# Kernel optimization log

Measured on AMD Instinct MI355X. Metric: run time of the kernel, lower is better.

Reference implementation:

```python
import jax, jax.numpy as jnp
import numpy as np

N, E, D = 50000, 800000, 128
EPS = 1e-5  # PyG BatchNorm default eps


def setup_inputs() -> dict:
    key = jax.random.key(0)
    ks = jax.random.split(key, 12)
    s = 1.0 / np.sqrt(D)
    x = jax.random.normal(ks[0], (N, D), jnp.float32)
    edge_index = jax.random.randint(ks[1], (2, E), 0, N, dtype=jnp.int32)
    Wp = jax.random.normal(ks[2], (D, D), jnp.float32) * s
    bp = jax.random.normal(ks[3], (D,), jnp.float32) * 0.01
    # 4 SAGEConv layers, all 128->128, stacked: lin_l (neighbor, with bias) and lin_r (root)
    Wl = jax.random.normal(ks[4], (4, D, D), jnp.float32) * s
    bl = jax.random.normal(ks[5], (4, D), jnp.float32) * 0.01
    Wr = jax.random.normal(ks[6], (4, D, D), jnp.float32) * s
    # BatchNorm params/buffers (eval mode: running stats)
    bn_gamma = 1.0 + 0.1 * jax.random.normal(ks[7], (4, D), jnp.float32)
    bn_beta = 0.1 * jax.random.normal(ks[8], (4, D), jnp.float32)
    bn_mean = 0.1 * jax.random.normal(ks[9], (4, D), jnp.float32)
    bn_var = jax.random.uniform(ks[10], (4, D), jnp.float32, 0.5, 1.5)
    return {"x": x, "edge_index": edge_index, "Wp": Wp, "bp": bp, "Wl": Wl,
            "bl": bl, "Wr": Wr, "bn_gamma": bn_gamma, "bn_beta": bn_beta,
            "bn_mean": bn_mean, "bn_var": bn_var}


def _sage_conv(x, src, dst, inv_deg, Wl, bl, Wr):
    # mean-aggregate neighbor features: gather x[src], scatter-sum to dst, divide by degree
    agg = jax.ops.segment_sum(x[src], dst, num_segments=N) * inv_deg  # [N, D]
    # PyG SAGEConv: lin_l(aggr) + lin_r(x_root)
    return agg @ Wl + bl + x @ Wr


def _bn(h, gamma, beta, mean, var):
    return (h - mean) * (gamma * jax.lax.rsqrt(var + EPS)) + beta


def reference(x, edge_index, Wp, bp, Wl, bl, Wr, bn_gamma, bn_beta, bn_mean, bn_var):
    src, dst = edge_index[0], edge_index[1]
    deg = jax.ops.segment_sum(jnp.ones((E,), x.dtype), dst, num_segments=N)
    inv_deg = (1.0 / jnp.maximum(deg, 1.0))[:, None]  # [N, 1]
    x = jax.nn.relu(x @ Wp + bp)
    # eval mode: dropout is identity, BN uses running stats
    for i in range(3):
        h = _sage_conv(x, src, dst, inv_deg, Wl[i], bl[i], Wr[i])
        h = jax.nn.relu(_bn(h, bn_gamma[i], bn_beta[i], bn_mean[i], bn_var[i]))
        x = x + h
    x = _sage_conv(x, src, dst, inv_deg, Wl[3], bl[3], Wr[3])
    return jax.nn.relu(_bn(x, bn_gamma[3], bn_beta[3], bn_mean[3], bn_var[3]))
```

## Files before the change

### kernel.cpp

```cpp
#include <hip/hip_runtime.h>

#define DIM 128
#define BN_EPS 1e-5f
#define BCAP 8192
#define EPB 4096
#define EPT 16

typedef __bf16 bf16x8 __attribute__((ext_vector_type(8)));
typedef float f32x4 __attribute__((ext_vector_type(4)));
typedef float f32x2 __attribute__((ext_vector_type(2)));

__device__ __forceinline__ float bf_e0(unsigned int u) {
    return __builtin_bit_cast(float, u << 16);
}
__device__ __forceinline__ float bf_e1(unsigned int u) {
    return __builtin_bit_cast(float, u & 0xffff0000u);
}
__device__ __forceinline__ unsigned short f2b(float f) {
    __bf16 b = (__bf16)f;
    return __builtin_bit_cast(unsigned short, b);
}
__device__ __forceinline__ unsigned int pack2(float lo, float hi) {
    return (unsigned int)f2b(lo) | ((unsigned int)f2b(hi) << 16);
}

#define GLOAD_LDS16(gsrc, ldst)                                               \
    __builtin_amdgcn_global_load_lds(                                         \
        (const __attribute__((address_space(1))) void*)(gsrc),                \
        (__attribute__((address_space(3))) void*)(ldst), 16, 0, 0)

__global__ __launch_bounds__(256) void k_bin(const int* __restrict__ src,
                                             const int* __restrict__ dst,
                                             int* __restrict__ cursor,
                                             unsigned int* __restrict__ binned,
                                             const float* __restrict__ Wp,
                                             const float* __restrict__ Wl,
                                             const float* __restrict__ Wr,
                                             unsigned short* __restrict__ WTf,
                                             int E, int NB) {
    __shared__ int hist[256];
    __shared__ int base[256];
    __shared__ int c2[256];
    const int tid = threadIdx.x;
    const int e0 = blockIdx.x * EPB;

    unsigned int u[EPT];
    int b[EPT];
    hist[tid] = 0;
    c2[tid] = 0;
    __syncthreads();
#pragma unroll
    for (int i = 0; i < EPT; ++i) {
        int e = e0 + i * 256 + tid;
        if (e < E) {
            int d = dst[e];
            b[i] = d >> 8;
            u[i] = ((unsigned int)(d & 255) << 17) | (unsigned int)src[e];
            atomicAdd(&hist[b[i]], 1);
        } else {
            b[i] = -1;
        }
    }
    __syncthreads();
    if (tid < NB && hist[tid] > 0) base[tid] = atomicAdd(&cursor[tid], hist[tid]);
    __syncthreads();
#pragma unroll
    for (int i = 0; i < EPT; ++i) {
        if (b[i] < 0) continue;
        int p = base[b[i]] + atomicAdd(&c2[b[i]], 1);
        if (p < BCAP) binned[(size_t)b[i] * BCAP + p] = u[i];
    }

    int gid = blockIdx.x * 256 + tid;
    if (gid < 9 * 2048) {
        int m = gid >> 11;
        int r = gid & 2047;
        int lane = r & 63;
        int k = (r >> 6) & 3;
        int ct = r >> 8;
        int feat = ct * 16 + (lane & 15);
        int kb = k * 32 + (lane >> 4) * 8;
        const float* W = (m == 0) ? Wp : (m < 5) ? (Wl + (size_t)(m - 1) * DIM * DIM)
                                                 : (Wr + (size_t)(m - 5) * DIM * DIM);
        unsigned short o[8];
#pragma unroll
        for (int e = 0; e < 8; ++e) o[e] = f2b(W[(size_t)(kb + e) * DIM + feat]);
        *(uint4*)(WTf + (size_t)gid * 8) = *(const uint4*)o;
    }
}

__global__ __launch_bounds__(256) void k_csr(const int* __restrict__ cursor,
                                             const unsigned int* __restrict__ binned,
                                             int* __restrict__ rowptr,
                                             float* __restrict__ inv_deg,
                                             int* __restrict__ col, int N, int NB) {
    __shared__ unsigned int stage[BCAP];
    __shared__ int deg[256];
    __shared__ int start[256];
    __shared__ int sh[256];
    const int b = blockIdx.x;
    const int t = threadIdx.x;
    const int node0 = b << 8;

    int v = (t < NB) ? min(cursor[t], BCAP) : 0;
    sh[t] = v;
    deg[t] = 0;
    __syncthreads();
    for (int off = 1; off < 256; off <<= 1) {
        int a = (t >= off) ? sh[t - off] : 0;
        __syncthreads();
        sh[t] += a;
        __syncthreads();
    }
    const int gbase = sh[b] - min(cursor[b], BCAP);
    const int cnt = min(cursor[b], BCAP);
    if (b == 0 && t == 255) rowptr[N] = sh[255];

    for (int e = t; e < cnt; e += 256) {
        unsigned int u = binned[(size_t)b * BCAP + e];
        stage[e] = u;
        atomicAdd(&deg[u >> 17], 1);
    }
    __syncthreads();
    int d = deg[t];
    start[t] = d;
    __syncthreads();
    for (int off = 1; off < 256; off <<= 1) {
        int a = (t >= off) ? start[t - off] : 0;
        __syncthreads();
        start[t] += a;
        __syncthreads();
    }
    int excl = start[t] - d;
    int node = node0 + t;
    if (node < N) {
        rowptr[node] = gbase + excl;
        inv_deg[node] = 1.0f / (float)(d > 1 ? d : 1);
    }
    __syncthreads();
    deg[t] = excl;
    __syncthreads();
    for (int e = t; e < cnt; e += 256) {
        unsigned int u = stage[e];
        int dl = u >> 17;
        int p = atomicAdd(&deg[dl], 1);
        col[gbase + p] = (int)(u & 0x1ffffu);
    }
}

__global__ void k_agg(const uint2* __restrict__ x8_2, const int* __restrict__ rowptr,
                      const int* __restrict__ col, const float* __restrict__ inv_deg,
                      uint4* __restrict__ aggb4, int n) {
    int node = (blockIdx.x * blockDim.x + threadIdx.x) >> 6;
    int lane = threadIdx.x & 63;
    if (node >= n) return;
    const int e4 = lane >> 4, c16 = lane & 15;
    const int lo = rowptr[node], hi = rowptr[node + 1];

    float a0 = 0.f, a1 = 0.f, a2 = 0.f, a3 = 0.f,
          a4 = 0.f, a5 = 0.f, a6 = 0.f, a7 = 0.f;

    int i0 = lo + e4;
    int s0 = (i0      < hi) ? col[i0]      : -1;
    int s1 = (i0 + 4  < hi) ? col[i0 + 4]  : -1;
    int s2 = (i0 + 8  < hi) ? col[i0 + 8]  : -1;
    int s3 = (i0 + 12 < hi) ? col[i0 + 12] : -1;

    for (int j = lo; j < hi; j += 16) {
        uint2 v0 = x8_2[(size_t)(s0 > 0 ? s0 : 0) * 16 + c16];
        uint2 v1 = x8_2[(size_t)(s1 > 0 ? s1 : 0) * 16 + c16];
        uint2 v2 = x8_2[(size_t)(s2 > 0 ? s2 : 0) * 16 + c16];
        uint2 v3 = x8_2[(size_t)(s3 > 0 ? s3 : 0) * 16 + c16];
        float m0 = s0 >= 0 ? 1.f : 0.f;
        float m1 = s1 >= 0 ? 1.f : 0.f;
        float m2 = s2 >= 0 ? 1.f : 0.f;
        float m3 = s3 >= 0 ? 1.f : 0.f;
        int nj = j + 16 + e4;
        s0 = (nj      < hi) ? col[nj]      : -1;
        s1 = (nj + 4  < hi) ? col[nj + 4]  : -1;
        s2 = (nj + 8  < hi) ? col[nj + 8]  : -1;
        s3 = (nj + 12 < hi) ? col[nj + 12] : -1;
#define ACC_(v, m)                                                            \
        {                                                                     \
            f32x2 f01 = __builtin_amdgcn_cvt_pk_f32_fp8(v.x, false);          \
            f32x2 f23 = __builtin_amdgcn_cvt_pk_f32_fp8(v.x, true);           \
            f32x2 f45 = __builtin_amdgcn_cvt_pk_f32_fp8(v.y, false);          \
            f32x2 f67 = __builtin_amdgcn_cvt_pk_f32_fp8(v.y, true);           \
            a0 = fmaf(f01.x, m, a0); a1 = fmaf(f01.y, m, a1);                 \
            a2 = fmaf(f23.x, m, a2); a3 = fmaf(f23.y, m, a3);                 \
            a4 = fmaf(f45.x, m, a4); a5 = fmaf(f45.y, m, a5);                 \
            a6 = fmaf(f67.x, m, a6); a7 = fmaf(f67.y, m, a7);                 \
        }
        ACC_(v0, m0) ACC_(v1, m1) ACC_(v2, m2) ACC_(v3, m3)
#undef ACC_
    }
#define RED_(a) a += __shfl_xor(a, 16); a += __shfl_xor(a, 32);
    RED_(a0) RED_(a1) RED_(a2) RED_(a3) RED_(a4) RED_(a5) RED_(a6) RED_(a7)
#undef RED_
    float sc = inv_deg[node];
    uint4 o;
    o.x = pack2(a0 * sc, a1 * sc);
    o.y = pack2(a2 * sc, a3 * sc);
    o.z = pack2(a4 * sc, a5 * sc);
    o.w = pack2(a6 * sc, a7 * sc);
    if (lane < 16) aggb4[(size_t)node * 16 + c16] = o;
}

template <int NSEG, bool A0F32>
__global__ __launch_bounds__(256) void k_gemm(
    const void* __restrict__ A0v, const unsigned short* __restrict__ A1,
    const unsigned short* __restrict__ Wf0, const unsigned short* __restrict__ Wf1,
    const float* __restrict__ bias,
    const float* __restrict__ gamma, const float* __restrict__ beta,
    const float* __restrict__ mean, const float* __restrict__ var,
    const unsigned short* __restrict__ residb,
    float* __restrict__ out32, unsigned short* __restrict__ outb,
    unsigned char* __restrict__ out8, int nrows) {
    __shared__ unsigned short wlds[16384];
    __shared__ float colp[2 * DIM];

    const int tid = threadIdx.x;
    const int lane = tid & 63;
    const int l15 = lane & 15;
    const int lhi = lane >> 4;
    const int wave = tid >> 6;
    const int node = blockIdx.x * 64 + wave * 16 + l15;
    const int arow = node < nrows ? node : nrows - 1;

    bf16x8 af0[4];
    if (A0F32) {
        const float* a0 = (const float*)A0v + (size_t)arow * DIM + lhi * 8;
#pragma unroll
        for (int k = 0; k < 4; ++k) {
            float4 v0 = *(const float4*)(a0 + k * 32);
            float4 v1 = *(const float4*)(a0 + k * 32 + 4);
            bf16x8 f;
            f[0] = (__bf16)v0.x; f[1] = (__bf16)v0.y;
            f[2] = (__bf16)v0.z; f[3] = (__bf16)v0.w;
            f[4] = (__bf16)v1.x; f[5] = (__bf16)v1.y;
            f[6] = (__bf16)v1.z; f[7] = (__bf16)v1.w;
            af0[k] = f;
        }
    } else {
        const unsigned short* a0 = (const unsigned short*)A0v + (size_t)arow * DIM + lhi * 8;
#pragma unroll
        for (int k = 0; k < 4; ++k) af0[k] = *(const bf16x8*)(a0 + k * 32);
    }

    {
        const unsigned short* g = Wf0 + (size_t)wave * 4096 + lane * 8;
#pragma unroll
        for (int i = 0; i < 8; ++i)
            GLOAD_LDS16(g + i * 512, &wlds[wave * 4096 + i * 512]);
    }

    if (tid < DIM) {
        float sc, sh;
        if (gamma) {
            float s = gamma[tid] * rsqrtf(var[tid] + BN_EPS);
            sc = s;
            sh = (bias[tid] - mean[tid]) * s + beta[tid];
        } else {
            sc = 1.f;
            sh = bias[tid];
        }
        colp[tid * 2] = sc;
        colp[tid * 2 + 1] = sh;
    }

    f32x4 acc[8];
#pragma unroll
    for (int ct = 0; ct < 8; ++ct) acc[ct] = (f32x4){0.f, 0.f, 0.f, 0.f};

    __syncthreads();

    bf16x8 af1[4];
    if (NSEG == 2) {
        const unsigned short* a1 = A1 + (size_t)arow * DIM + lhi * 8;
#pragma unroll
        for (int k = 0; k < 4; ++k) af1[k] = *(const bf16x8*)(a1 + k * 32);
    }

#pragma unroll
    for (int k = 0; k < 4; ++k) {
        bf16x8 bw[8];
#pragma unroll
        for (int ct = 0; ct < 8; ++ct)
            bw[ct] = *(const bf16x8*)&wlds[((ct * 4 + k) * 64 + lane) * 8];
#pragma unroll
        for (int ct = 0; ct < 8; ++ct)
            acc[ct] = __builtin_amdgcn_mfma_f32_16x16x32_bf16(bw[ct], af0[k],
                                                              acc[ct], 0, 0, 0);
    }

    if (NSEG == 2) {
        __syncthreads();
        {
            const unsigned short* g = Wf1 + (size_t)wave * 4096 + lane * 8;
#pragma unroll
            for (int i = 0; i < 8; ++i)
                GLOAD_LDS16(g + i * 512, &wlds[wave * 4096 + i * 512]);
        }
        __syncthreads();
#pragma unroll
        for (int k = 0; k < 4; ++k) {
            bf16x8 bw[8];
#pragma unroll
            for (int ct = 0; ct < 8; ++ct)
                bw[ct] = *(const bf16x8*)&wlds[((ct * 4 + k) * 64 + lane) * 8];
#pragma unroll
            for (int ct = 0; ct < 8; ++ct)
                acc[ct] = __builtin_amdgcn_mfma_f32_16x16x32_bf16(bw[ct], af1[k],
                                                                  acc[ct], 0, 0, 0);
        }
    }

    if (node < nrows) {
#pragma unroll
        for (int ct = 0; ct < 8; ++ct) {
            int c0 = ct * 16 + lhi * 4;
            float h[4];
#pragma unroll
            for (int j = 0; j < 4; ++j) {
                float2 p = *(const float2*)&colp[(c0 + j) * 2];
                h[j] = fmaxf(acc[ct][j] * p.x + p.y, 0.f);
            }
            size_t base = (size_t)node * DIM + c0;
            if (residb) {
                uint2 rv = *(const uint2*)(residb + base);
                h[0] += bf_e0(rv.x); h[1] += bf_e1(rv.x);
                h[2] += bf_e0(rv.y); h[3] += bf_e1(rv.y);
            }
            if (outb) {
                uint2 o;
                o.x = pack2(h[0], h[1]);
                o.y = pack2(h[2], h[3]);
                *(uint2*)(outb + base) = o;
            }
            if (out8) {
                int w = __builtin_amdgcn_cvt_pk_fp8_f32(h[0], h[1], 0, false);
                w = __builtin_amdgcn_cvt_pk_fp8_f32(h[2], h[3], w, true);
                *(unsigned int*)(out8 + base) = (unsigned int)w;
            }
            if (out32)
                *(float4*)(out32 + base) = make_float4(h[0], h[1], h[2], h[3]);
        }
    }
}

extern "C" void kernel_launch(void* const* d_in, const int* in_sizes, int n_in,
                              void* d_out, int out_size, void* d_ws, size_t ws_size,
                              hipStream_t stream) {
    const float* x_in = (const float*)d_in[0];
    const int* ei     = (const int*)d_in[1];
    const float* Wp   = (const float*)d_in[2];
    const float* bp   = (const float*)d_in[3];
    const float* Wl   = (const float*)d_in[4];
    const float* bl   = (const float*)d_in[5];
    const float* Wr   = (const float*)d_in[6];
    const float* g    = (const float*)d_in[7];
    const float* be   = (const float*)d_in[8];
    const float* mu   = (const float*)d_in[9];
    const float* va   = (const float*)d_in[10];

    const int N = in_sizes[0] / DIM;
    const int E = in_sizes[1] / 2;
    const int* src = ei;
    const int* dst = ei + E;
    const int NB = (N + 255) >> 8;

    char* p = (char*)d_ws;
    auto alloc = [&](size_t bytes) {
        char* r = p;
        p += (bytes + 255) & ~(size_t)255;
        return r;
    };
    float* inv_deg = (float*)alloc((size_t)N * 4);
    int* rowptr    = (int*)alloc((size_t)(N + 1) * 4);
    int* cursor    = (int*)alloc((size_t)NB * 4);
    int* col       = (int*)alloc((size_t)E * 4);
    unsigned int* binned = (unsigned int*)alloc((size_t)NB * BCAP * 4);
    unsigned short* xb   = (unsigned short*)alloc((size_t)N * DIM * 2);
    unsigned char* x8    = (unsigned char*)alloc((size_t)N * DIM);
    unsigned short* aggb = (unsigned short*)alloc((size_t)N * DIM * 2);
    unsigned short* WTf  = (unsigned short*)alloc((size_t)9 * 16384 * 2);

    hipMemsetAsync(cursor, 0, (size_t)NB * 4, stream);
    k_bin<<<(E + EPB - 1) / EPB, 256, 0, stream>>>(src, dst, cursor, binned,
                                                   Wp, Wl, Wr, WTf, E, NB);
    k_csr<<<NB, 256, 0, stream>>>(cursor, binned, rowptr, inv_deg, col, N, NB);

    const int gblocks = (N + 63) / 64;

    k_gemm<1, true><<<gblocks, 256, 0, stream>>>(
        x_in, nullptr, WTf, nullptr, bp,
        nullptr, nullptr, nullptr, nullptr, nullptr,
        nullptr, xb, x8, N);

    float* out = (float*)d_out;
    for (int i = 0; i < 4; ++i) {
        k_agg<<<(N + 3) / 4, 256, 0, stream>>>((const uint2*)x8, rowptr, col,
                                               inv_deg, (uint4*)aggb, N);
        const unsigned short* WlF = WTf + (size_t)(1 + i) * 16384;
        const unsigned short* WrF = WTf + (size_t)(5 + i) * 16384;
        k_gemm<2, false><<<gblocks, 256, 0, stream>>>(
            aggb, xb, WlF, WrF, bl + i * DIM,
            g + i * DIM, be + i * DIM, mu + i * DIM, va + i * DIM,
            (i < 3) ? xb : nullptr,
            (i < 3) ? nullptr : out, (i < 3) ? xb : nullptr,
            (i < 3) ? x8 : nullptr, N);
    }
}
```

Measured before the change: 209.6 us.

## Fuse neighbor aggregation into per-layer SAGE GEMM kernel with ping-pong fp8 buffers

Replaces the separate aggregation kernel and two-segment GEMM with one per-layer kernel. Each wave first gathers and mean-aggregates 16 nodes, two at a time, into a swizzled LDS tile, then runs the Wl and Wr MFMAs. Weights are read straight from global memory instead of being staged in LDS. This removes the bf16 aggregate round-trip to memory and one launch per layer, and the fp8 feature buffer is now double-buffered to avoid a read-write race. The cost is far fewer waves for the latency-bound gather (16 nodes per wave instead of one), plus possible imbalance from pairing nodes of different degree.

Result: slower. 318.3 us (+51.8%).

```diff
diff --git a/kernel.cpp b/kernel.cpp
--- a/kernel.cpp
+++ b/kernel.cpp
@@ -148,76 +148,12 @@
     }
 }
 
-__global__ void k_agg(const uint2* __restrict__ x8_2, const int* __restrict__ rowptr,
-                      const int* __restrict__ col, const float* __restrict__ inv_deg,
-                      uint4* __restrict__ aggb4, int n) {
-    int node = (blockIdx.x * blockDim.x + threadIdx.x) >> 6;
-    int lane = threadIdx.x & 63;
-    if (node >= n) return;
-    const int e4 = lane >> 4, c16 = lane & 15;
-    const int lo = rowptr[node], hi = rowptr[node + 1];
-
-    float a0 = 0.f, a1 = 0.f, a2 = 0.f, a3 = 0.f,
-          a4 = 0.f, a5 = 0.f, a6 = 0.f, a7 = 0.f;
-
-    int i0 = lo + e4;
-    int s0 = (i0      < hi) ? col[i0]      : -1;
-    int s1 = (i0 + 4  < hi) ? col[i0 + 4]  : -1;
-    int s2 = (i0 + 8  < hi) ? col[i0 + 8]  : -1;
-    int s3 = (i0 + 12 < hi) ? col[i0 + 12] : -1;
-
-    for (int j = lo; j < hi; j += 16) {
-        uint2 v0 = x8_2[(size_t)(s0 > 0 ? s0 : 0) * 16 + c16];
-        uint2 v1 = x8_2[(size_t)(s1 > 0 ? s1 : 0) * 16 + c16];
-        uint2 v2 = x8_2[(size_t)(s2 > 0 ? s2 : 0) * 16 + c16];
-        uint2 v3 = x8_2[(size_t)(s3 > 0 ? s3 : 0) * 16 + c16];
-        float m0 = s0 >= 0 ? 1.f : 0.f;
-        float m1 = s1 >= 0 ? 1.f : 0.f;
-        float m2 = s2 >= 0 ? 1.f : 0.f;
-        float m3 = s3 >= 0 ? 1.f : 0.f;
-        int nj = j + 16 + e4;
-        s0 = (nj      < hi) ? col[nj]      : -1;
-        s1 = (nj + 4  < hi) ? col[nj + 4]  : -1;
-        s2 = (nj + 8  < hi) ? col[nj + 8]  : -1;
-        s3 = (nj + 12 < hi) ? col[nj + 12] : -1;
-#define ACC_(v, m)                                                            \
-        {                                                                     \
-            f32x2 f01 = __builtin_amdgcn_cvt_pk_f32_fp8(v.x, false);          \
-            f32x2 f23 = __builtin_amdgcn_cvt_pk_f32_fp8(v.x, true);           \
-            f32x2 f45 = __builtin_amdgcn_cvt_pk_f32_fp8(v.y, false);          \
-            f32x2 f67 = __builtin_amdgcn_cvt_pk_f32_fp8(v.y, true);           \
-            a0 = fmaf(f01.x, m, a0); a1 = fmaf(f01.y, m, a1);                 \
-            a2 = fmaf(f23.x, m, a2); a3 = fmaf(f23.y, m, a3);                 \
-            a4 = fmaf(f45.x, m, a4); a5 = fmaf(f45.y, m, a5);                 \
-            a6 = fmaf(f67.x, m, a6); a7 = fmaf(f67.y, m, a7);                 \
-        }
-        ACC_(v0, m0) ACC_(v1, m1) ACC_(v2, m2) ACC_(v3, m3)
-#undef ACC_
-    }
-#define RED_(a) a += __shfl_xor(a, 16); a += __shfl_xor(a, 32);
-    RED_(a0) RED_(a1) RED_(a2) RED_(a3) RED_(a4) RED_(a5) RED_(a6) RED_(a7)
-#undef RED_
-    float sc = inv_deg[node];
-    uint4 o;
-    o.x = pack2(a0 * sc, a1 * sc);
-    o.y = pack2(a2 * sc, a3 * sc);
-    o.z = pack2(a4 * sc, a5 * sc);
-    o.w = pack2(a6 * sc, a7 * sc);
-    if (lane < 16) aggb4[(size_t)node * 16 + c16] = o;
-}
-
-template <int NSEG, bool A0F32>
-__global__ __launch_bounds__(256) void k_gemm(
-    const void* __restrict__ A0v, const unsigned short* __restrict__ A1,
-    const unsigned short* __restrict__ Wf0, const unsigned short* __restrict__ Wf1,
+__global__ __launch_bounds__(256) void k_proj(
+    const float* __restrict__ Ain, const unsigned short* __restrict__ Wf,
     const float* __restrict__ bias,
-    const float* __restrict__ gamma, const float* __restrict__ beta,
-    const float* __restrict__ mean, const float* __restrict__ var,
-    const unsigned short* __restrict__ residb,
-    float* __restrict__ out32, unsigned short* __restrict__ outb,
-    unsigned char* __restrict__ out8, int nrows) {
+    unsigned short* __restrict__ outb, unsigned char* __restrict__ out8,
+    int nrows) {
     __shared__ unsigned short wlds[16384];
-    __shared__ float colp[2 * DIM];
 
     const int tid = threadIdx.x;
     const int lane = tid & 63;
@@ -227,9 +163,9 @@
     const int node = blockIdx.x * 64 + wave * 16 + l15;
     const int arow = node < nrows ? node : nrows - 1;
 
-    bf16x8 af0[4];
-    if (A0F32) {
-        const float* a0 = (const float*)A0v + (size_t)arow * DIM + lhi * 8;
+    bf16x8 af[4];
+    {
+        const float* a0 = Ain + (size_t)arow * DIM + lhi * 8;
 #pragma unroll
         for (int k = 0; k < 4; ++k) {
             float4 v0 = *(const float4*)(a0 + k * 32);
@@ -239,47 +175,21 @@
             f[2] = (__bf16)v0.z; f[3] = (__bf16)v0.w;
             f[4] = (__bf16)v1.x; f[5] = (__bf16)v1.y;
             f[6] = (__bf16)v1.z; f[7] = (__bf16)v1.w;
-            af0[k] = f;
-        }
-    } else {
-        const unsigned short* a0 = (const unsigned short*)A0v + (size_t)arow * DIM + lhi * 8;
-#pragma unroll
-        for (int k = 0; k < 4; ++k) af0[k] = *(const bf16x8*)(a0 + k * 32);
-    }
-
+            af[k] = f;
+        }
+    }
     {
-        const unsigned short* g = Wf0 + (size_t)wave * 4096 + lane * 8;
+        const unsigned short* g = Wf + (size_t)wave * 4096 + lane * 8;
 #pragma unroll
         for (int i = 0; i < 8; ++i)
             GLOAD_LDS16(g + i * 512, &wlds[wave * 4096 + i * 512]);
     }
 
-    if (tid < DIM) {
-        float sc, sh;
-        if (gamma) {
-            float s = gamma[tid] * rsqrtf(var[tid] + BN_EPS);
-            sc = s;
-            sh = (bias[tid] - mean[tid]) * s + beta[tid];
-        } else {
-            sc = 1.f;
-            sh = bias[tid];
-        }
-        colp[tid * 2] = sc;
-        colp[tid * 2 + 1] = sh;
-    }
-
     f32x4 acc[8];
 #pragma unroll
     for (int ct = 0; ct < 8; ++ct) acc[ct] = (f32x4){0.f, 0.f, 0.f, 0.f};
 
     __syncthreads();
-
-    bf16x8 af1[4];
-    if (NSEG == 2) {
-        const unsigned short* a1 = A1 + (size_t)arow * DIM + lhi * 8;
-#pragma unroll
-        for (int k = 0; k < 4; ++k) af1[k] = *(const bf16x8*)(a1 + k * 32);
-    }
 
 #pragma unroll
     for (int k = 0; k < 4; ++k) {
@@ -289,33 +199,179 @@
             bw[ct] = *(const bf16x8*)&wlds[((ct * 4 + k) * 64 + lane) * 8];
 #pragma unroll
         for (int ct = 0; ct < 8; ++ct)
+            acc[ct] = __builtin_amdgcn_mfma_f32_16x16x32_bf16(bw[ct], af[k],
+                                                              acc[ct], 0, 0, 0);
+    }
+
+    if (node < nrows) {
+#pragma unroll
+        for (int ct = 0; ct < 8; ++ct) {
+            int c0 = ct * 16 + lhi * 4;
+            float4 bb = *(const float4*)(bias + c0);
+            float h[4];
+            h[0] = fmaxf(acc[ct][0] + bb.x, 0.f);
+            h[1] = fmaxf(acc[ct][1] + bb.y, 0.f);
+            h[2] = fmaxf(acc[ct][2] + bb.z, 0.f);
+            h[3] = fmaxf(acc[ct][3] + bb.w, 0.f);
+            size_t base = (size_t)node * DIM + c0;
+            uint2 o;
+            o.x = pack2(h[0], h[1]);
+            o.y = pack2(h[2], h[3]);
+            *(uint2*)(outb + base) = o;
+            int w = __builtin_amdgcn_cvt_pk_fp8_f32(h[0], h[1], 0, false);
+            w = __builtin_amdgcn_cvt_pk_fp8_f32(h[2], h[3], w, true);
+            *(unsigned int*)(out8 + base) = (unsigned int)w;
+        }
+    }
+}
+
+__global__ __launch_bounds__(256) void k_layer(
+    const uint2* __restrict__ x8in, const unsigned short* __restrict__ xb,
+    const int* __restrict__ rowptr, const int* __restrict__ col,
+    const float* __restrict__ inv_deg,
+    const unsigned short* __restrict__ Wl, const unsigned short* __restrict__ Wr,
+    const float* __restrict__ bias, const float* __restrict__ gamma,
+    const float* __restrict__ beta, const float* __restrict__ mean,
+    const float* __restrict__ var,
+    unsigned short* __restrict__ outb, unsigned char* __restrict__ out8,
+    float* __restrict__ out32, int nrows) {
+    __shared__ uint4 atile[4][16][16];
+    __shared__ float colp[2 * DIM];
+
+    const int tid = threadIdx.x;
+    const int lane = tid & 63;
+    const int wave = tid >> 6;
+    const int l15 = lane & 15;
+    const int lhi = lane >> 4;
+    const int e4 = lhi, c16 = l15;
+    const int nbase = blockIdx.x * 64 + wave * 16;
+
+    if (tid < DIM) {
+        float s = gamma[tid] * rsqrtf(var[tid] + BN_EPS);
+        colp[tid * 2] = s;
+        colp[tid * 2 + 1] = (bias[tid] - mean[tid]) * s + beta[tid];
+    }
+
+#define PRIME4(S0, S1, S2, S3, base_, hi_)                                    \
+    S0 = ((base_) < (hi_)) ? col[(base_)] : -1;                               \
+    S1 = ((base_) + 4 < (hi_)) ? col[(base_) + 4] : -1;                       \
+    S2 = ((base_) + 8 < (hi_)) ? col[(base_) + 8] : -1;                       \
+    S3 = ((base_) + 12 < (hi_)) ? col[(base_) + 12] : -1;
+
+#define CVT8ACC(v, m, Q0, Q1, Q2, Q3, Q4, Q5, Q6, Q7)                         \
+    {                                                                         \
+        f32x2 f01 = __builtin_amdgcn_cvt_pk_f32_fp8((v).x, false);            \
+        f32x2 f23 = __builtin_amdgcn_cvt_pk_f32_fp8((v).x, true);             \
+        f32x2 f45 = __builtin_amdgcn_cvt_pk_f32_fp8((v).y, false);            \
+        f32x2 f67 = __builtin_amdgcn_cvt_pk_f32_fp8((v).y, true);             \
+        Q0 = fmaf(f01.x, m, Q0); Q1 = fmaf(f01.y, m, Q1);                     \
+        Q2 = fmaf(f23.x, m, Q2); Q3 = fmaf(f23.y, m, Q3);                     \
+        Q4 = fmaf(f45.x, m, Q4); Q5 = fmaf(f45.y, m, Q5);                     \
+        Q6 = fmaf(f67.x, m, Q6); Q7 = fmaf(f67.y, m, Q7);                     \
+    }
+
+#define RED2(q) q += __shfl_xor(q, 16); q += __shfl_xor(q, 32);
+
+    for (int i = 0; i < 16; i += 2) {
+        const int nA = nbase + i, nB = nbase + i + 1;
+        float A0 = 0.f, A1 = 0.f, A2 = 0.f, A3 = 0.f,
+              A4 = 0.f, A5 = 0.f, A6 = 0.f, A7 = 0.f;
+        float B0 = 0.f, B1 = 0.f, B2 = 0.f, B3 = 0.f,
+              B4 = 0.f, B5 = 0.f, B6 = 0.f, B7 = 0.f;
+        int loA = 0, hiA = 0, loB = 0, hiB = 0;
+        if (nA < nrows) { loA = rowptr[nA]; hiA = rowptr[nA + 1]; }
+        if (nB < nrows) { loB = rowptr[nB]; hiB = rowptr[nB + 1]; }
+        int sA0, sA1, sA2, sA3, sB0, sB1, sB2, sB3;
+        PRIME4(sA0, sA1, sA2, sA3, loA + e4, hiA)
+        PRIME4(sB0, sB1, sB2, sB3, loB + e4, hiB)
+        for (int jA = loA, jB = loB; jA < hiA || jB < hiB; jA += 16, jB += 16) {
+            uint2 vA0 = x8in[(size_t)(sA0 > 0 ? sA0 : 0) * 16 + c16];
+            uint2 vA1 = x8in[(size_t)(sA1 > 0 ? sA1 : 0) * 16 + c16];
+            uint2 vA2 = x8in[(size_t)(sA2 > 0 ? sA2 : 0) * 16 + c16];
+            uint2 vA3 = x8in[(size_t)(sA3 > 0 ? sA3 : 0) * 16 + c16];
+            uint2 vB0 = x8in[(size_t)(sB0 > 0 ? sB0 : 0) * 16 + c16];
+            uint2 vB1 = x8in[(size_t)(sB1 > 0 ? sB1 : 0) * 16 + c16];
+            uint2 vB2 = x8in[(size_t)(sB2 > 0 ? sB2 : 0) * 16 + c16];
+            uint2 vB3 = x8in[(size_t)(sB3 > 0 ? sB3 : 0) * 16 + c16];
+            float mA0 = sA0 >= 0 ? 1.f : 0.f, mA1 = sA1 >= 0 ? 1.f : 0.f;
+            float mA2 = sA2 >= 0 ? 1.f : 0.f, mA3 = sA3 >= 0 ? 1.f : 0.f;
+            float mB0 = sB0 >= 0 ? 1.f : 0.f, mB1 = sB1 >= 0 ? 1.f : 0.f;
+            float mB2 = sB2 >= 0 ? 1.f : 0.f, mB3 = sB3 >= 0 ? 1.f : 0.f;
+            PRIME4(sA0, sA1, sA2, sA3, jA + 16 + e4, hiA)
+            PRIME4(sB0, sB1, sB2, sB3, jB + 16 + e4, hiB)
+            CVT8ACC(vA0, mA0, A0, A1, A2, A3, A4, A5, A6, A7)
+            CVT8ACC(vA1, mA1, A0, A1, A2, A3, A4, A5, A6, A7)
+            CVT8ACC(vA2, mA2, A0, A1, A2, A3, A4, A5, A6, A7)
+            CVT8ACC(vA3, mA3, A0, A1, A2, A3, A4, A5, A6, A7)
+            CVT8ACC(vB0, mB0, B0, B1, B2, B3, B4, B5, B6, B7)
+            CVT8ACC(vB1, mB1, B0, B1, B2, B3, B4, B5, B6, B7)
+            CVT8ACC(vB2, mB2, B0, B1, B2, B3, B4, B5, B6, B7)
+            CVT8ACC(vB3, mB3, B0, B1, B2, B3, B4, B5, B6, B7)
+        }
+        RED2(A0) RED2(A1) RED2(A2) RED2(A3) RED2(A4) RED2(A5) RED2(A6) RED2(A7)
+        RED2(B0) RED2(B1) RED2(B2) RED2(B3) RED2(B4) RED2(B5) RED2(B6) RED2(B7)
+        if (lane < 16) {
+            float scA = (nA < nrows) ? inv_deg[nA] : 0.f;
+            float scB = (nB < nrows) ? inv_deg[nB] : 0.f;
+            uint4 oA, oB;
+            oA.x = pack2(A0 * scA, A1 * scA);
+            oA.y = pack2(A2 * scA, A3 * scA);
+            oA.z = pack2(A4 * scA, A5 * scA);
+            oA.w = pack2(A6 * scA, A7 * scA);
+            oB.x = pack2(B0 * scB, B1 * scB);
+            oB.y = pack2(B2 * scB, B3 * scB);
+            oB.z = pack2(B4 * scB, B5 * scB);
+            oB.w = pack2(B6 * scB, B7 * scB);
+            atile[wave][i][c16 ^ i] = oA;
+            atile[wave][i + 1][c16 ^ (i + 1)] = oB;
+        }
+    }
+#undef PRIME4
+#undef CVT8ACC
+#undef RED2
+
+    const int gnode = nbase + l15;
+    const int arow = gnode < nrows ? gnode : nrows - 1;
+    bf16x8 af1[4];
+#pragma unroll
+    for (int k = 0; k < 4; ++k)
+        af1[k] = *(const bf16x8*)(xb + (size_t)arow * DIM + k * 32 + lhi * 8);
+
+    __syncthreads();
+
+    bf16x8 af0[4];
+#pragma unroll
+    for (int k = 0; k < 4; ++k)
+        af0[k] = __builtin_bit_cast(bf16x8, atile[wave][l15][(k * 4 + lhi) ^ l15]);
+
+    f32x4 acc[8];
+#pragma unroll
+    for (int ct = 0; ct < 8; ++ct) acc[ct] = (f32x4){0.f, 0.f, 0.f, 0.f};
+
+#pragma unroll
+    for (int k = 0; k < 4; ++k) {
+        bf16x8 bw[8];
+#pragma unroll
+        for (int ct = 0; ct < 8; ++ct)
+            bw[ct] = *(const bf16x8*)(Wl + ((size_t)(ct * 4 + k) * 64 + lane) * 8);
+#pragma unroll
+        for (int ct = 0; ct < 8; ++ct)
             acc[ct] = __builtin_amdgcn_mfma_f32_16x16x32_bf16(bw[ct], af0[k],
                                                               acc[ct], 0, 0, 0);
     }
-
-    if (NSEG == 2) {
-        __syncthreads();
-        {
-            const unsigned short* g = Wf1 + (size_t)wave * 4096 + lane * 8;
-#pragma unroll
-            for (int i = 0; i < 8; ++i)
-                GLOAD_LDS16(g + i * 512, &wlds[wave * 4096 + i * 512]);
-        }
-        __syncthreads();
-#pragma unroll
-        for (int k = 0; k < 4; ++k) {
-            bf16x8 bw[8];
-#pragma unroll
-            for (int ct = 0; ct < 8; ++ct)
-                bw[ct] = *(const bf16x8*)&wlds[((ct * 4 + k) * 64 + lane) * 8];
-#pragma unroll
-            for (int ct = 0; ct < 8; ++ct)
-                acc[ct] = __builtin_amdgcn_mfma_f32_16x16x32_bf16(bw[ct], af1[k],
-                                                                  acc[ct], 0, 0, 0);
-        }
-    }
-
-    if (node < nrows) {
+#pragma unroll
+    for (int k = 0; k < 4; ++k) {
+        bf16x8 bw[8];
+#pragma unroll
+        for (int ct = 0; ct < 8; ++ct)
+            bw[ct] = *(const bf16x8*)(Wr + ((size_t)(ct * 4 + k) * 64 + lane) * 8);
+#pragma unroll
+        for (int ct = 0; ct < 8; ++ct)
+            acc[ct] = __builtin_amdgcn_mfma_f32_16x16x32_bf16(bw[ct], af1[k],
+                                                              acc[ct], 0, 0, 0);
+    }
+
+    if (gnode < nrows) {
 #pragma unroll
         for (int ct = 0; ct < 8; ++ct) {
             int c0 = ct * 16 + lhi * 4;
@@ -325,19 +381,15 @@
                 float2 p = *(const float2*)&colp[(c0 + j) * 2];
                 h[j] = fmaxf(acc[ct][j] * p.x + p.y, 0.f);
             }
-            size_t base = (size_t)node * DIM + c0;
-            if (residb) {
-                uint2 rv = *(const uint2*)(residb + base);
+            size_t base = (size_t)gnode * DIM + c0;
+            if (outb) {
+                uint2 rv = *(const uint2*)(xb + base);
                 h[0] += bf_e0(rv.x); h[1] += bf_e1(rv.x);
                 h[2] += bf_e0(rv.y); h[3] += bf_e1(rv.y);
-            }
-            if (outb) {
                 uint2 o;
                 o.x = pack2(h[0], h[1]);
                 o.y = pack2(h[2], h[3]);
                 *(uint2*)(outb + base) = o;
-            }
-            if (out8) {
                 int w = __builtin_amdgcn_cvt_pk_fp8_f32(h[0], h[1], 0, false);
                 w = __builtin_amdgcn_cvt_pk_fp8_f32(h[2], h[3], w, true);
                 *(unsigned int*)(out8 + base) = (unsigned int)w;
@@ -381,8 +433,8 @@
     int* col       = (int*)alloc((size_t)E * 4);
     unsigned int* binned = (unsigned int*)alloc((size_t)NB * BCAP * 4);
     unsigned short* xb   = (unsigned short*)alloc((size_t)N * DIM * 2);
-    unsigned char* x8    = (unsigned char*)alloc((size_t)N * DIM);
-    unsigned short* aggb = (unsigned short*)alloc((size_t)N * DIM * 2);
+    unsigned char* x8a   = (unsigned char*)alloc((size_t)N * DIM);
+    unsigned char* x8b   = (unsigned char*)alloc((size_t)N * DIM);
     unsigned short* WTf  = (unsigned short*)alloc((size_t)9 * 16384 * 2);
 
     hipMemsetAsync(cursor, 0, (size_t)NB * 4, stream);
@@ -392,22 +444,20 @@
 
     const int gblocks = (N + 63) / 64;
 
-    k_gemm<1, true><<<gblocks, 256, 0, stream>>>(
-        x_in, nullptr, WTf, nullptr, bp,
-        nullptr, nullptr, nullptr, nullptr, nullptr,
-        nullptr, xb, x8, N);
+    k_proj<<<gblocks, 256, 0, stream>>>(x_in, WTf, bp, xb, x8a, N);
 
     float* out = (float*)d_out;
+    unsigned char* x8rd = x8a;
+    unsigned char* x8wr = x8b;
     for (int i = 0; i < 4; ++i) {
-        k_agg<<<(N + 3) / 4, 256, 0, stream>>>((const uint2*)x8, rowptr, col,
-                                               inv_deg, (uint4*)aggb, N);
         const unsigned short* WlF = WTf + (size_t)(1 + i) * 16384;
         const unsigned short* WrF = WTf + (size_t)(5 + i) * 16384;
-        k_gemm<2, false><<<gblocks, 256, 0, stream>>>(
-            aggb, xb, WlF, WrF, bl + i * DIM,
-            g + i * DIM, be + i * DIM, mu + i * DIM, va + i * DIM,
-            (i < 3) ? xb : nullptr,
-            (i < 3) ? nullptr : out, (i < 3) ? xb : nullptr,
-            (i < 3) ? x8 : nullptr, N);
-    }
-}
+        const bool last = (i == 3);
+        k_layer<<<gblocks, 256, 0, stream>>>(
+            (const uint2*)x8rd, xb, rowptr, col, inv_deg, WlF, WrF,
+            bl + i * DIM, g + i * DIM, be + i * DIM, mu + i * DIM, va + i * DIM,
+            last ? nullptr : xb, last ? nullptr : x8wr,
+            last ? out : nullptr, N);
+        unsigned char* t = x8rd; x8rd = x8wr; x8wr = t;
+    }
+}
```
